# Kernel optimization log

Hardware: AMD Instinct MI355X
Metric: run time of the kernel (lower is better)

The kernel has to match this reference:

```python
import jax, jax.numpy as jnp
import numpy as np

NU, NV, D, H, E = 100000, 50000, 128, 128, 1600000
ALPHA = 0.2  # LeakyReLU slope


def _spmm(rows, cols, vals, x, n_rows):
    # sparse [n_rows, n_cols] @ dense [n_cols, d] via gather + segment_sum
    return jax.ops.segment_sum(vals[:, None] * x[cols], rows, num_segments=n_rows)


def _gcn(x, rows, cols, vals, n_rows, W, b):
    support = x @ W + b  # bias added before spmm is equivalent only if... original adds after spmm
    return None


def _gcn_layer(x, rows, cols, vals, n_rows, W, b):
    support = x @ W
    out = _spmm(rows, cols, vals, support, n_rows) + b
    return jnp.where(out >= 0, out, ALPHA * out)  # LeakyReLU


def _reparam(mean, logstd, noise):
    sigma = jnp.exp(0.1 + 0.9 * jax.nn.softplus(logstd))
    return noise * sigma + mean


def setup_inputs() -> dict:
    key = jax.random.key(0)
    ks = jax.random.split(key, 24)
    stdv = 1.0 / np.sqrt(H)
    u = lambda k, shp, s: jax.random.uniform(k, shp, jnp.float32, -s, s)
    inp = {
        "ufea": jax.random.normal(ks[0], (NU, D), jnp.float32),
        "vfea": jax.random.normal(ks[1], (NV, D), jnp.float32),
        "uv_rows": jax.random.randint(ks[2], (E,), 0, NU, jnp.int32),
        "uv_cols": jax.random.randint(ks[3], (E,), 0, NV, jnp.int32),
        "uv_vals": jax.random.uniform(ks[4], (E,), jnp.float32),
        "vu_rows": jax.random.randint(ks[5], (E,), 0, NV, jnp.int32),
        "vu_cols": jax.random.randint(ks[6], (E,), 0, NU, jnp.int32),
        "vu_vals": jax.random.uniform(ks[7], (E,), jnp.float32),
        "noise_u": jax.random.normal(ks[8], (NU, H), jnp.float32),
        "noise_v": jax.random.normal(ks[9], (NV, H), jnp.float32),
        "gc1_W": u(ks[10], (D, H), stdv), "gc1_b": u(ks[11], (H,), stdv),
        "gc3m_W": u(ks[12], (H, H), stdv), "gc3m_b": u(ks[13], (H,), stdv),
        "gc3s_W": u(ks[14], (H, H), stdv), "gc3s_b": u(ks[15], (H,), stdv),
        "um_W": u(ks[16], (2 * H, H), stdv), "um_b": u(ks[17], (H,), stdv),
        "us_W": u(ks[18], (2 * H, H), stdv), "us_b": u(ks[19], (H,), stdv),
        "im_W": u(ks[20], (2 * H, H), stdv), "im_b": u(ks[21], (H,), stdv),
        "is_W": u(ks[22], (2 * H, H), stdv), "is_b": u(ks[23], (H,), stdv),
    }
    return inp


def reference(ufea, vfea, uv_rows, uv_cols, uv_vals, vu_rows, vu_cols, vu_vals,
              noise_u, noise_v, gc1_W, gc1_b, gc3m_W, gc3m_b, gc3s_W, gc3s_b,
              um_W, um_b, us_W, us_b, im_W, im_b, is_W, is_b):
    nu, nv = ufea.shape[0], vfea.shape[0]
    # user path: VU_adj [nv, nu] then UV_adj [nu, nv]
    user_ho = _gcn_layer(ufea, vu_rows, vu_cols, vu_vals, nv, gc1_W, gc1_b)        # [nv, H]
    user_ho_mean = _gcn_layer(user_ho, uv_rows, uv_cols, uv_vals, nu, gc3m_W, gc3m_b)  # [nu, H]
    user_ho_logstd = _gcn_layer(user_ho, uv_rows, uv_cols, uv_vals, nu, gc3s_W, gc3s_b)
    user_mean = jnp.concatenate((user_ho_mean, ufea), axis=1) @ um_W + um_b
    user_logstd = jnp.concatenate((user_ho_logstd, ufea), axis=1) @ us_W + us_b
    user_z = _reparam(user_mean, user_logstd, noise_u)
    # item path: UV_adj [nu, nv] then VU_adj [nv, nu]
    item_ho = _gcn_layer(vfea, uv_rows, uv_cols, uv_vals, nu, gc1_W, gc1_b)        # [nu, H]
    item_ho_mean = _gcn_layer(item_ho, vu_rows, vu_cols, vu_vals, nv, gc3m_W, gc3m_b)  # [nv, H]
    item_ho_logstd = _gcn_layer(item_ho, vu_rows, vu_cols, vu_vals, nv, gc3s_W, gc3s_b)
    item_mean = jnp.concatenate((item_ho_mean, vfea), axis=1) @ im_W + im_b
    item_logstd = jnp.concatenate((item_ho_logstd, vfea), axis=1) @ is_W + is_b
    item_z = _reparam(item_mean, item_logstd, noise_v)
    return user_z, item_z
```

## Files before the change

kernel.cpp:

```cpp
#include <hip/hip_runtime.h>
#include <math.h>

typedef float f32x4 __attribute__((ext_vector_type(4)));
typedef __bf16 bf16x8 __attribute__((ext_vector_type(8)));
typedef __bf16 bf16x4 __attribute__((ext_vector_type(4)));

#define LRELU_ALPHA 0.2f

__global__ void edge_count(const int* __restrict__ rows, int* __restrict__ cnt, int E) {
    int i = blockIdx.x * 256 + threadIdx.x;
    if (i < E) atomicAdd(&cnt[rows[i]], 1);
}

__global__ __launch_bounds__(512) void scan1(const int* __restrict__ in, int* __restrict__ out,
                                             int* __restrict__ bsum, int ncnt, int nout) {
    __shared__ int s[512];
    int t = threadIdx.x;
    int i = blockIdx.x * 512 + t;
    int v = (i < ncnt) ? in[i] : 0;
    s[t] = v; __syncthreads();
    for (int o = 1; o < 512; o <<= 1) {
        int u = (t >= o) ? s[t - o] : 0;
        __syncthreads();
        s[t] += u;
        __syncthreads();
    }
    if (i < nout) out[i] = s[t] - v;
    if (t == 511) bsum[blockIdx.x] = s[511];
}

__global__ void scan2(int* __restrict__ b, int nb) {
    __shared__ int s[256];
    int t = threadIdx.x;
    int v = (t < nb) ? b[t] : 0;
    s[t] = v; __syncthreads();
    for (int o = 1; o < 256; o <<= 1) {
        int u = (t >= o) ? s[t - o] : 0;
        __syncthreads();
        s[t] += u;
        __syncthreads();
    }
    if (t < nb) b[t] = s[t] - v;
}

__global__ __launch_bounds__(512) void scan3(int* __restrict__ out, const int* __restrict__ bsum, int nout) {
    int i = blockIdx.x * 512 + threadIdx.x;
    if (i < nout) out[i] += bsum[blockIdx.x];
}

__global__ void edge_fill(const int* __restrict__ rows, const int* __restrict__ cols,
                          const float* __restrict__ vals, int* __restrict__ cur,
                          int* __restrict__ ocol, float* __restrict__ oval, int E) {
    int i = blockIdx.x * 256 + threadIdx.x;
    if (i < E) {
        int r = rows[i];
        int p = atomicAdd(&cur[r], 1);
        ocol[p] = cols[i];
        oval[p] = vals[i];
    }
}

__global__ void prep_wt(const float* __restrict__ W, unsigned short* __restrict__ Whi,
                        unsigned short* __restrict__ Wlo, int K) {
    int i = blockIdx.x * 256 + threadIdx.x;
    if (i < K * 128) {
        int k = i >> 7, n = i & 127;
        float f = W[i];
        __bf16 h = (__bf16)f;
        __bf16 l = (__bf16)(f - (float)h);
        Whi[n * K + k] = __builtin_bit_cast(unsigned short, h);
        Wlo[n * K + k] = __builtin_bit_cast(unsigned short, l);
    }
}

__global__ __launch_bounds__(256) void spmm_lrelu(const int* __restrict__ ptr, const int* __restrict__ cols,
                                                  const float* __restrict__ vals, const float* __restrict__ x,
                                                  const float* __restrict__ bias, float* __restrict__ out,
                                                  int nrows) {
    int w = (blockIdx.x << 2) + (threadIdx.x >> 6);
    if (w >= nrows) return;
    int lane = threadIdx.x & 63;
    int s = ptr[w], e = ptr[w + 1];
    const float2* __restrict__ x2 = (const float2*)x;
    float ax = 0.f, ay = 0.f;
    int i = s;
    for (; i + 3 < e; i += 4) {
        int c0 = cols[i], c1 = cols[i + 1], c2 = cols[i + 2], c3 = cols[i + 3];
        float v0 = vals[i], v1 = vals[i + 1], v2 = vals[i + 2], v3 = vals[i + 3];
        float2 g0 = x2[(size_t)c0 * 64 + lane];
        float2 g1 = x2[(size_t)c1 * 64 + lane];
        float2 g2 = x2[(size_t)c2 * 64 + lane];
        float2 g3 = x2[(size_t)c3 * 64 + lane];
        ax += v0 * g0.x + v1 * g1.x + v2 * g2.x + v3 * g3.x;
        ay += v0 * g0.y + v1 * g1.y + v2 * g2.y + v3 * g3.y;
    }
    for (; i < e; i++) {
        int c = cols[i]; float v = vals[i];
        float2 g = x2[(size_t)c * 64 + lane];
        ax += v * g.x; ay += v * g.y;
    }
    float2 b2 = ((const float2*)bias)[lane];
    ax += b2.x; ay += b2.y;
    ax = ax >= 0.f ? ax : LRELU_ALPHA * ax;
    ay = ay >= 0.f ? ay : LRELU_ALPHA * ay;
    float2 o; o.x = ax; o.y = ay;
    ((float2*)out)[(size_t)w * 64 + lane] = o;
}

template <int KT, int EPI>
__global__ __launch_bounds__(256) void gemm128(const float* __restrict__ A1, const float* __restrict__ A2,
                                               const unsigned short* __restrict__ Whi,
                                               const unsigned short* __restrict__ Wlo,
                                               const float* __restrict__ bias,
                                               const float* __restrict__ noise,
                                               float* C, int M) {
    constexpr int K = KT * 64;
    __shared__ __bf16 Ahi[128][72];
    __shared__ __bf16 Alo[128][72];
    __shared__ __bf16 Bhi[128][72];
    __shared__ __bf16 Blo[128][72];
    const int t = threadIdx.x;
    const int lane = t & 63;
    const int w = t >> 6;
    const int wr = w >> 1, wc = w & 1;
    const int l15 = lane & 15, l4 = lane >> 4;
    const int row0 = blockIdx.x * 128;

    f32x4 acc[4][4] = {};

    for (int k0 = 0; k0 < K; k0 += 64) {
        __syncthreads();
        {
            int r = t >> 1, half = t & 1;
            int rg = row0 + r;
            const float* src;
            if constexpr (KT == 2) {
                src = A1 + (size_t)rg * 128 + k0;
            } else {
                src = (k0 < 128) ? (A1 + (size_t)rg * 128 + k0)
                                 : (A2 + (size_t)rg * 128 + (k0 - 128));
            }
#pragma unroll
            for (int q = 0; q < 8; q++) {
                int kk = half * 32 + 4 * q;
                float4 f;
                if (rg < M) f = *(const float4*)(src + kk);
                else        f = make_float4(0.f, 0.f, 0.f, 0.f);
                bf16x4 h, l;
                h[0] = (__bf16)f.x; l[0] = (__bf16)(f.x - (float)h[0]);
                h[1] = (__bf16)f.y; l[1] = (__bf16)(f.y - (float)h[1]);
                h[2] = (__bf16)f.z; l[2] = (__bf16)(f.z - (float)h[2]);
                h[3] = (__bf16)f.w; l[3] = (__bf16)(f.w - (float)h[3]);
                *(bf16x4*)&Ahi[r][kk] = h;
                *(bf16x4*)&Alo[r][kk] = l;
            }
            int n = t >> 1;
            const unsigned short* whsrc = Whi + (size_t)n * K + k0 + half * 32;
            const unsigned short* wlsrc = Wlo + (size_t)n * K + k0 + half * 32;
#pragma unroll
            for (int q = 0; q < 4; q++) {
                uint4 uh = *(const uint4*)(whsrc + 8 * q);
                uint4 ul = *(const uint4*)(wlsrc + 8 * q);
                *(uint4*)&Bhi[n][half * 32 + 8 * q] = uh;
                *(uint4*)&Blo[n][half * 32 + 8 * q] = ul;
            }
        }
        __syncthreads();
#pragma unroll
        for (int kh = 0; kh < 2; kh++) {
            bf16x8 ah[4], al[4], bh[4], bl[4];
#pragma unroll
            for (int mr = 0; mr < 4; mr++) {
                ah[mr] = *(const bf16x8*)&Ahi[wr * 64 + mr * 16 + l15][kh * 32 + l4 * 8];
                al[mr] = *(const bf16x8*)&Alo[wr * 64 + mr * 16 + l15][kh * 32 + l4 * 8];
            }
#pragma unroll
            for (int nc = 0; nc < 4; nc++) {
                bh[nc] = *(const bf16x8*)&Bhi[wc * 64 + nc * 16 + l15][kh * 32 + l4 * 8];
                bl[nc] = *(const bf16x8*)&Blo[wc * 64 + nc * 16 + l15][kh * 32 + l4 * 8];
            }
#pragma unroll
            for (int mr = 0; mr < 4; mr++)
#pragma unroll
                for (int nc = 0; nc < 4; nc++) {
                    acc[mr][nc] = __builtin_amdgcn_mfma_f32_16x16x32_bf16(ah[mr], bh[nc], acc[mr][nc], 0, 0, 0);
                    acc[mr][nc] = __builtin_amdgcn_mfma_f32_16x16x32_bf16(ah[mr], bl[nc], acc[mr][nc], 0, 0, 0);
                    acc[mr][nc] = __builtin_amdgcn_mfma_f32_16x16x32_bf16(al[mr], bh[nc], acc[mr][nc], 0, 0, 0);
                }
        }
    }

#pragma unroll
    for (int mr = 0; mr < 4; mr++) {
        int rowb = row0 + wr * 64 + mr * 16 + l4 * 4;
#pragma unroll
        for (int nc = 0; nc < 4; nc++) {
            int col = wc * 64 + nc * 16 + l15;
#pragma unroll
            for (int j = 0; j < 4; j++) {
                int r = rowb + j;
                if (r < M) {
                    float v = acc[mr][nc][j];
                    if constexpr (EPI == 0) {
                        C[(size_t)r * 128 + col] = v;
                    } else if constexpr (EPI == 1) {
                        C[(size_t)r * 128 + col] = v + bias[col];
                    } else {
                        float mean = v + bias[col];
                        float ls = C[(size_t)r * 128 + col];
                        float sp = ls > 0.f ? ls + log1pf(expf(-ls)) : log1pf(expf(ls));
                        float sg = expf(0.1f + 0.9f * sp);
                        C[(size_t)r * 128 + col] = noise[(size_t)r * 128 + col] * sg + mean;
                    }
                }
            }
        }
    }
}

extern "C" void kernel_launch(void* const* d_in, const int* in_sizes, int n_in,
                              void* d_out, int out_size, void* d_ws, size_t ws_size,
                              hipStream_t stream) {
    const float* ufea    = (const float*)d_in[0];
    const float* vfea    = (const float*)d_in[1];
    const int*   uv_rows = (const int*)d_in[2];
    const int*   uv_cols = (const int*)d_in[3];
    const float* uv_vals = (const float*)d_in[4];
    const int*   vu_rows = (const int*)d_in[5];
    const int*   vu_cols = (const int*)d_in[6];
    const float* vu_vals = (const float*)d_in[7];
    const float* noise_u = (const float*)d_in[8];
    const float* noise_v = (const float*)d_in[9];
    const float* gc1_W  = (const float*)d_in[10];
    const float* gc1_b  = (const float*)d_in[11];
    const float* gc3m_W = (const float*)d_in[12];
    const float* gc3m_b = (const float*)d_in[13];
    const float* gc3s_W = (const float*)d_in[14];
    const float* gc3s_b = (const float*)d_in[15];
    const float* um_W = (const float*)d_in[16];
    const float* um_b = (const float*)d_in[17];
    const float* us_W = (const float*)d_in[18];
    const float* us_b = (const float*)d_in[19];
    const float* im_W = (const float*)d_in[20];
    const float* im_b = (const float*)d_in[21];
    const float* is_W = (const float*)d_in[22];
    const float* is_b = (const float*)d_in[23];

    const int H  = in_sizes[11];
    const int D  = in_sizes[10] / H;
    const int NU = in_sizes[0] / D;
    const int NV = in_sizes[1] / D;
    const int E  = in_sizes[2];

    char* ws = (char*)d_ws;
    size_t off = 0;
    auto alloc = [&](size_t bytes) -> char* {
        char* p = ws + off;
        off = (off + bytes + 255) & ~(size_t)255;
        return p;
    };
    unsigned short* wt_gc1_h  = (unsigned short*)alloc(128 * 128 * 2);
    unsigned short* wt_gc1_l  = (unsigned short*)alloc(128 * 128 * 2);
    unsigned short* wt_gc3m_h = (unsigned short*)alloc(128 * 128 * 2);
    unsigned short* wt_gc3m_l = (unsigned short*)alloc(128 * 128 * 2);
    unsigned short* wt_gc3s_h = (unsigned short*)alloc(128 * 128 * 2);
    unsigned short* wt_gc3s_l = (unsigned short*)alloc(128 * 128 * 2);
    unsigned short* wt_um_h = (unsigned short*)alloc(128 * 256 * 2);
    unsigned short* wt_um_l = (unsigned short*)alloc(128 * 256 * 2);
    unsigned short* wt_us_h = (unsigned short*)alloc(128 * 256 * 2);
    unsigned short* wt_us_l = (unsigned short*)alloc(128 * 256 * 2);
    unsigned short* wt_im_h = (unsigned short*)alloc(128 * 256 * 2);
    unsigned short* wt_im_l = (unsigned short*)alloc(128 * 256 * 2);
    unsigned short* wt_is_h = (unsigned short*)alloc(128 * 256 * 2);
    unsigned short* wt_is_l = (unsigned short*)alloc(128 * 256 * 2);
    int*   ptr_uv = (int*)alloc((size_t)(NU + 1) * 4);
    int*   cur_uv = (int*)alloc((size_t)NU * 4);
    int*   col_uv = (int*)alloc((size_t)E * 4);
    float* val_uv = (float*)alloc((size_t)E * 4);
    int*   ptr_vu = (int*)alloc((size_t)(NV + 1) * 4);
    int*   cur_vu = (int*)alloc((size_t)NV * 4);
    int*   col_vu = (int*)alloc((size_t)E * 4);
    float* val_vu = (float*)alloc((size_t)E * 4);
    int*   bsum   = (int*)alloc(1024 * 4);
    float* bufA = (float*)alloc((size_t)NU * 128 * 4);
    float* bufB = (float*)alloc((size_t)NU * 128 * 4);

    float* outU = (float*)d_out;
    float* outI = outU + (size_t)NU * H;

    const int eb = (E + 255) / 256;
    const int nbU = (NU + 1 + 511) / 512;
    const int nbV = (NV + 1 + 511) / 512;
    const int gU = (NU + 127) / 128, gV = (NV + 127) / 128;
    const int sU = (NU + 3) / 4, sV = (NV + 3) / 4;

    hipMemsetAsync(cur_uv, 0, (size_t)NU * 4, stream);
    hipMemsetAsync(cur_vu, 0, (size_t)NV * 4, stream);
    edge_count<<<eb, 256, 0, stream>>>(uv_rows, cur_uv, E);
    edge_count<<<eb, 256, 0, stream>>>(vu_rows, cur_vu, E);
    scan1<<<nbU, 512, 0, stream>>>(cur_uv, ptr_uv, bsum, NU, NU + 1);
    scan2<<<1, 256, 0, stream>>>(bsum, nbU);
    scan3<<<nbU, 512, 0, stream>>>(ptr_uv, bsum, NU + 1);
    scan1<<<nbV, 512, 0, stream>>>(cur_vu, ptr_vu, bsum, NV, NV + 1);
    scan2<<<1, 256, 0, stream>>>(bsum, nbV);
    scan3<<<nbV, 512, 0, stream>>>(ptr_vu, bsum, NV + 1);
    hipMemcpyAsync(cur_uv, ptr_uv, (size_t)NU * 4, hipMemcpyDeviceToDevice, stream);
    hipMemcpyAsync(cur_vu, ptr_vu, (size_t)NV * 4, hipMemcpyDeviceToDevice, stream);
    edge_fill<<<eb, 256, 0, stream>>>(uv_rows, uv_cols, uv_vals, cur_uv, col_uv, val_uv, E);
    edge_fill<<<eb, 256, 0, stream>>>(vu_rows, vu_cols, vu_vals, cur_vu, col_vu, val_vu, E);

    prep_wt<<<64, 256, 0, stream>>>(gc1_W, wt_gc1_h, wt_gc1_l, 128);
    prep_wt<<<64, 256, 0, stream>>>(gc3m_W, wt_gc3m_h, wt_gc3m_l, 128);
    prep_wt<<<64, 256, 0, stream>>>(gc3s_W, wt_gc3s_h, wt_gc3s_l, 128);
    prep_wt<<<128, 256, 0, stream>>>(um_W, wt_um_h, wt_um_l, 256);
    prep_wt<<<128, 256, 0, stream>>>(us_W, wt_us_h, wt_us_l, 256);
    prep_wt<<<128, 256, 0, stream>>>(im_W, wt_im_h, wt_im_l, 256);
    prep_wt<<<128, 256, 0, stream>>>(is_W, wt_is_h, wt_is_l, 256);

    gemm128<2, 0><<<gU, 256, 0, stream>>>(ufea, nullptr, wt_gc1_h, wt_gc1_l, nullptr, nullptr, bufA, NU);
    spmm_lrelu<<<sV, 256, 0, stream>>>(ptr_vu, col_vu, val_vu, bufA, gc1_b, bufB, NV);
    gemm128<2, 0><<<gV, 256, 0, stream>>>(bufB, nullptr, wt_gc3s_h, wt_gc3s_l, nullptr, nullptr, bufA, NV);
    spmm_lrelu<<<sU, 256, 0, stream>>>(ptr_uv, col_uv, val_uv, bufA, gc3s_b, outU, NU);
    gemm128<4, 1><<<gU, 256, 0, stream>>>(outU, ufea, wt_us_h, wt_us_l, us_b, nullptr, outU, NU);
    gemm128<2, 0><<<gV, 256, 0, stream>>>(bufB, nullptr, wt_gc3m_h, wt_gc3m_l, nullptr, nullptr, bufA, NV);
    spmm_lrelu<<<sU, 256, 0, stream>>>(ptr_uv, col_uv, val_uv, bufA, gc3m_b, bufB, NU);
    gemm128<4, 2><<<gU, 256, 0, stream>>>(bufB, ufea, wt_um_h, wt_um_l, um_b, noise_u, outU, NU);

    gemm128<2, 0><<<gV, 256, 0, stream>>>(vfea, nullptr, wt_gc1_h, wt_gc1_l, nullptr, nullptr, bufA, NV);
    spmm_lrelu<<<sU, 256, 0, stream>>>(ptr_uv, col_uv, val_uv, bufA, gc1_b, bufB, NU);
    gemm128<2, 0><<<gU, 256, 0, stream>>>(bufB, nullptr, wt_gc3s_h, wt_gc3s_l, nullptr, nullptr, bufA, NU);
    spmm_lrelu<<<sV, 256, 0, stream>>>(ptr_vu, col_vu, val_vu, bufA, gc3s_b, outI, NV);
    gemm128<4, 1><<<gV, 256, 0, stream>>>(outI, vfea, wt_is_h, wt_is_l, is_b, nullptr, outI, NV);
    gemm128<2, 0><<<gU, 256, 0, stream>>>(bufB, nullptr, wt_gc3m_h, wt_gc3m_l, nullptr, nullptr, bufA, NU);
    spmm_lrelu<<<sV, 256, 0, stream>>>(ptr_vu, col_vu, val_vu, bufA, gc3m_b, bufB, NV);
    gemm128<4, 2><<<gV, 256, 0, stream>>>(bufB, vfea, wt_im_h, wt_im_l, im_b, noise_v, outI, NV);

    (void)n_in; (void)out_size; (void)ws_size;
}
```

Before: 1.802 ms.

## Replace LDS-tiled GEMM with register-direct MFMA using pre-swizzled weight fragments

Weights are pre-arranged into MFMA fragment order so each lane loads its B operand straight from global memory. The A operand is likewise loaded per lane directly into registers, which removes all shared-memory staging and block barriers. Each wave now computes 32 rows by all 128 columns instead of a 64x64 tile. This drops LDS traffic and syncs, at the cost of redundant weight loads per wave (served from cache) and less coalesced A loads.

```diff
diff --git a/kernel.cpp b/kernel.cpp
--- a/kernel.cpp
+++ b/kernel.cpp
@@ -3,7 +3,6 @@
 
 typedef float f32x4 __attribute__((ext_vector_type(4)));
 typedef __bf16 bf16x8 __attribute__((ext_vector_type(8)));
-typedef __bf16 bf16x4 __attribute__((ext_vector_type(4)));
 
 #define LRELU_ALPHA 0.2f
 
@@ -60,17 +59,21 @@
     }
 }
 
-__global__ void prep_wt(const float* __restrict__ W, unsigned short* __restrict__ Whi,
-                        unsigned short* __restrict__ Wlo, int K) {
-    int i = blockIdx.x * 256 + threadIdx.x;
-    if (i < K * 128) {
-        int k = i >> 7, n = i & 127;
-        float f = W[i];
-        __bf16 h = (__bf16)f;
-        __bf16 l = (__bf16)(f - (float)h);
-        Whi[n * K + k] = __builtin_bit_cast(unsigned short, h);
-        Wlo[n * K + k] = __builtin_bit_cast(unsigned short, l);
-    }
+__global__ void prep_frag(const float* __restrict__ W, unsigned short* __restrict__ Fh,
+                          unsigned short* __restrict__ Fl, int K) {
+    int o = blockIdx.x * 256 + threadIdx.x;
+    if (o >= K * 128) return;
+    int j = o & 7;
+    int lane = (o >> 3) & 63;
+    int blk = o >> 9;
+    int nc = blk & 7, kh = blk >> 3;
+    int col = nc * 16 + (lane & 15);
+    int k = kh * 32 + (lane >> 4) * 8 + j;
+    float f = W[k * 128 + col];
+    __bf16 h = (__bf16)f;
+    __bf16 l = (__bf16)(f - (float)h);
+    Fh[o] = __builtin_bit_cast(unsigned short, h);
+    Fl[o] = __builtin_bit_cast(unsigned short, l);
 }
 
 __global__ __launch_bounds__(256) void spmm_lrelu(const int* __restrict__ ptr, const int* __restrict__ cols,
@@ -107,95 +110,74 @@
     ((float2*)out)[(size_t)w * 64 + lane] = o;
 }
 
-template <int KT, int EPI>
-__global__ __launch_bounds__(256) void gemm128(const float* __restrict__ A1, const float* __restrict__ A2,
-                                               const unsigned short* __restrict__ Whi,
-                                               const unsigned short* __restrict__ Wlo,
-                                               const float* __restrict__ bias,
-                                               const float* __restrict__ noise,
-                                               float* C, int M) {
-    constexpr int K = KT * 64;
-    __shared__ __bf16 Ahi[128][72];
-    __shared__ __bf16 Alo[128][72];
-    __shared__ __bf16 Bhi[128][72];
-    __shared__ __bf16 Blo[128][72];
+template <int KPH, int EPI>
+__global__ __launch_bounds__(256) void gemm_reg(const float* __restrict__ A1, const float* __restrict__ A2,
+                                                const unsigned short* __restrict__ Fh,
+                                                const unsigned short* __restrict__ Fl,
+                                                const float* __restrict__ bias,
+                                                const float* __restrict__ noise,
+                                                float* __restrict__ C, int M) {
     const int t = threadIdx.x;
     const int lane = t & 63;
     const int w = t >> 6;
-    const int wr = w >> 1, wc = w & 1;
     const int l15 = lane & 15, l4 = lane >> 4;
-    const int row0 = blockIdx.x * 128;
-
-    f32x4 acc[4][4] = {};
-
-    for (int k0 = 0; k0 < K; k0 += 64) {
-        __syncthreads();
-        {
-            int r = t >> 1, half = t & 1;
-            int rg = row0 + r;
-            const float* src;
-            if constexpr (KT == 2) {
-                src = A1 + (size_t)rg * 128 + k0;
+    const int row0 = blockIdx.x * 128 + w * 32;
+
+    f32x4 acc[2][8] = {};
+
+#pragma unroll
+    for (int kh = 0; kh < KPH; kh++) {
+        const float* Asrc;
+        int kk;
+        if constexpr (KPH == 8) {
+            Asrc = (kh < 4) ? A1 : A2;
+            kk = (kh & 3) * 32 + l4 * 8;
+        } else {
+            Asrc = A1;
+            kk = kh * 32 + l4 * 8;
+        }
+        bf16x8 ah[2], al[2];
+#pragma unroll
+        for (int mr = 0; mr < 2; mr++) {
+            int r = row0 + mr * 16 + l15;
+            float4 f0, f1;
+            if (r < M) {
+                const float* p = Asrc + (size_t)r * 128 + kk;
+                f0 = *(const float4*)p;
+                f1 = *(const float4*)(p + 4);
             } else {
-                src = (k0 < 128) ? (A1 + (size_t)rg * 128 + k0)
-                                 : (A2 + (size_t)rg * 128 + (k0 - 128));
+                f0 = make_float4(0.f, 0.f, 0.f, 0.f);
+                f1 = f0;
             }
-#pragma unroll
-            for (int q = 0; q < 8; q++) {
-                int kk = half * 32 + 4 * q;
-                float4 f;
-                if (rg < M) f = *(const float4*)(src + kk);
-                else        f = make_float4(0.f, 0.f, 0.f, 0.f);
-                bf16x4 h, l;
-                h[0] = (__bf16)f.x; l[0] = (__bf16)(f.x - (float)h[0]);
-                h[1] = (__bf16)f.y; l[1] = (__bf16)(f.y - (float)h[1]);
-                h[2] = (__bf16)f.z; l[2] = (__bf16)(f.z - (float)h[2]);
-                h[3] = (__bf16)f.w; l[3] = (__bf16)(f.w - (float)h[3]);
-                *(bf16x4*)&Ahi[r][kk] = h;
-                *(bf16x4*)&Alo[r][kk] = l;
-            }
-            int n = t >> 1;
-            const unsigned short* whsrc = Whi + (size_t)n * K + k0 + half * 32;
-            const unsigned short* wlsrc = Wlo + (size_t)n * K + k0 + half * 32;
-#pragma unroll
-            for (int q = 0; q < 4; q++) {
-                uint4 uh = *(const uint4*)(whsrc + 8 * q);
-                uint4 ul = *(const uint4*)(wlsrc + 8 * q);
-                *(uint4*)&Bhi[n][half * 32 + 8 * q] = uh;
-                *(uint4*)&Blo[n][half * 32 + 8 * q] = ul;
+            float fv[8] = {f0.x, f0.y, f0.z, f0.w, f1.x, f1.y, f1.z, f1.w};
+#pragma unroll
+            for (int j = 0; j < 8; j++) {
+                __bf16 h = (__bf16)fv[j];
+                ah[mr][j] = h;
+                al[mr][j] = (__bf16)(fv[j] - (float)h);
             }
         }
-        __syncthreads();
-#pragma unroll
-        for (int kh = 0; kh < 2; kh++) {
-            bf16x8 ah[4], al[4], bh[4], bl[4];
-#pragma unroll
-            for (int mr = 0; mr < 4; mr++) {
-                ah[mr] = *(const bf16x8*)&Ahi[wr * 64 + mr * 16 + l15][kh * 32 + l4 * 8];
-                al[mr] = *(const bf16x8*)&Alo[wr * 64 + mr * 16 + l15][kh * 32 + l4 * 8];
+        const unsigned short* bh_base = Fh + (size_t)kh * 4096;
+        const unsigned short* bl_base = Fl + (size_t)kh * 4096;
+#pragma unroll
+        for (int nc = 0; nc < 8; nc++) {
+            bf16x8 bh = *(const bf16x8*)(bh_base + nc * 512 + lane * 8);
+            bf16x8 bl = *(const bf16x8*)(bl_base + nc * 512 + lane * 8);
+#pragma unroll
+            for (int mr = 0; mr < 2; mr++) {
+                acc[mr][nc] = __builtin_amdgcn_mfma_f32_16x16x32_bf16(ah[mr], bh, acc[mr][nc], 0, 0, 0);
+                acc[mr][nc] = __builtin_amdgcn_mfma_f32_16x16x32_bf16(ah[mr], bl, acc[mr][nc], 0, 0, 0);
+                acc[mr][nc] = __builtin_amdgcn_mfma_f32_16x16x32_bf16(al[mr], bh, acc[mr][nc], 0, 0, 0);
             }
-#pragma unroll
-            for (int nc = 0; nc < 4; nc++) {
-                bh[nc] = *(const bf16x8*)&Bhi[wc * 64 + nc * 16 + l15][kh * 32 + l4 * 8];
-                bl[nc] = *(const bf16x8*)&Blo[wc * 64 + nc * 16 + l15][kh * 32 + l4 * 8];
-            }
-#pragma unroll
-            for (int mr = 0; mr < 4; mr++)
-#pragma unroll
-                for (int nc = 0; nc < 4; nc++) {
-                    acc[mr][nc] = __builtin_amdgcn_mfma_f32_16x16x32_bf16(ah[mr], bh[nc], acc[mr][nc], 0, 0, 0);
-                    acc[mr][nc] = __builtin_amdgcn_mfma_f32_16x16x32_bf16(ah[mr], bl[nc], acc[mr][nc], 0, 0, 0);
-                    acc[mr][nc] = __builtin_amdgcn_mfma_f32_16x16x32_bf16(al[mr], bh[nc], acc[mr][nc], 0, 0, 0);
-                }
         }
     }
 
 #pragma unroll
-    for (int mr = 0; mr < 4; mr++) {
-        int rowb = row0 + wr * 64 + mr * 16 + l4 * 4;
-#pragma unroll
-        for (int nc = 0; nc < 4; nc++) {
-            int col = wc * 64 + nc * 16 + l15;
+    for (int mr = 0; mr < 2; mr++) {
+        int rowb = row0 + mr * 16 + l4 * 4;
+#pragma unroll
+        for (int nc = 0; nc < 8; nc++) {
+            int col = nc * 16 + l15;
 #pragma unroll
             for (int j = 0; j < 4; j++) {
                 int r = rowb + j;
@@ -259,20 +241,20 @@
         off = (off + bytes + 255) & ~(size_t)255;
         return p;
     };
-    unsigned short* wt_gc1_h  = (unsigned short*)alloc(128 * 128 * 2);
-    unsigned short* wt_gc1_l  = (unsigned short*)alloc(128 * 128 * 2);
-    unsigned short* wt_gc3m_h = (unsigned short*)alloc(128 * 128 * 2);
-    unsigned short* wt_gc3m_l = (unsigned short*)alloc(128 * 128 * 2);
-    unsigned short* wt_gc3s_h = (unsigned short*)alloc(128 * 128 * 2);
-    unsigned short* wt_gc3s_l = (unsigned short*)alloc(128 * 128 * 2);
-    unsigned short* wt_um_h = (unsigned short*)alloc(128 * 256 * 2);
-    unsigned short* wt_um_l = (unsigned short*)alloc(128 * 256 * 2);
-    unsigned short* wt_us_h = (unsigned short*)alloc(128 * 256 * 2);
-    unsigned short* wt_us_l = (unsigned short*)alloc(128 * 256 * 2);
-    unsigned short* wt_im_h = (unsigned short*)alloc(128 * 256 * 2);
-    unsigned short* wt_im_l = (unsigned short*)alloc(128 * 256 * 2);
-    unsigned short* wt_is_h = (unsigned short*)alloc(128 * 256 * 2);
-    unsigned short* wt_is_l = (unsigned short*)alloc(128 * 256 * 2);
+    unsigned short* wf_gc1_h  = (unsigned short*)alloc(128 * 128 * 2);
+    unsigned short* wf_gc1_l  = (unsigned short*)alloc(128 * 128 * 2);
+    unsigned short* wf_gc3m_h = (unsigned short*)alloc(128 * 128 * 2);
+    unsigned short* wf_gc3m_l = (unsigned short*)alloc(128 * 128 * 2);
+    unsigned short* wf_gc3s_h = (unsigned short*)alloc(128 * 128 * 2);
+    unsigned short* wf_gc3s_l = (unsigned short*)alloc(128 * 128 * 2);
+    unsigned short* wf_um_h = (unsigned short*)alloc(256 * 128 * 2);
+    unsigned short* wf_um_l = (unsigned short*)alloc(256 * 128 * 2);
+    unsigned short* wf_us_h = (unsigned short*)alloc(256 * 128 * 2);
+    unsigned short* wf_us_l = (unsigned short*)alloc(256 * 128 * 2);
+    unsigned short* wf_im_h = (unsigned short*)alloc(256 * 128 * 2);
+    unsigned short* wf_im_l = (unsigned short*)alloc(256 * 128 * 2);
+    unsigned short* wf_is_h = (unsigned short*)alloc(256 * 128 * 2);
+    unsigned short* wf_is_l = (unsigned short*)alloc(256 * 128 * 2);
     int*   ptr_uv = (int*)alloc((size_t)(NU + 1) * 4);
     int*   cur_uv = (int*)alloc((size_t)NU * 4);
     int*   col_uv = (int*)alloc((size_t)E * 4);
@@ -309,31 +291,31 @@
     edge_fill<<<eb, 256, 0, stream>>>(uv_rows, uv_cols, uv_vals, cur_uv, col_uv, val_uv, E);
     edge_fill<<<eb, 256, 0, stream>>>(vu_rows, vu_cols, vu_vals, cur_vu, col_vu, val_vu, E);
 
-    prep_wt<<<64, 256, 0, stream>>>(gc1_W, wt_gc1_h, wt_gc1_l, 128);
-    prep_wt<<<64, 256, 0, stream>>>(gc3m_W, wt_gc3m_h, wt_gc3m_l, 128);
-    prep_wt<<<64, 256, 0, stream>>>(gc3s_W, wt_gc3s_h, wt_gc3s_l, 128);
-    prep_wt<<<128, 256, 0, stream>>>(um_W, wt_um_h, wt_um_l, 256);
-    prep_wt<<<128, 256, 0, stream>>>(us_W, wt_us_h, wt_us_l, 256);
-    prep_wt<<<128, 256, 0, stream>>>(im_W, wt_im_h, wt_im_l, 256);
-    prep_wt<<<128, 256, 0, stream>>>(is_W, wt_is_h, wt_is_l, 256);
-
-    gemm128<2, 0><<<gU, 256, 0, stream>>>(ufea, nullptr, wt_gc1_h, wt_gc1_l, nullptr, nullptr, bufA, NU);
+    prep_frag<<<64, 256, 0, stream>>>(gc1_W, wf_gc1_h, wf_gc1_l, 128);
+    prep_frag<<<64, 256, 0, stream>>>(gc3m_W, wf_gc3m_h, wf_gc3m_l, 128);
+    prep_frag<<<64, 256, 0, stream>>>(gc3s_W, wf_gc3s_h, wf_gc3s_l, 128);
+    prep_frag<<<128, 256, 0, stream>>>(um_W, wf_um_h, wf_um_l, 256);
+    prep_frag<<<128, 256, 0, stream>>>(us_W, wf_us_h, wf_us_l, 256);
+    prep_frag<<<128, 256, 0, stream>>>(im_W, wf_im_h, wf_im_l, 256);
+    prep_frag<<<128, 256, 0, stream>>>(is_W, wf_is_h, wf_is_l, 256);
+
+    gemm_reg<4, 0><<<gU, 256, 0, stream>>>(ufea, nullptr, wf_gc1_h, wf_gc1_l, nullptr, nullptr, bufA, NU);
     spmm_lrelu<<<sV, 256, 0, stream>>>(ptr_vu, col_vu, val_vu, bufA, gc1_b, bufB, NV);
-    gemm128<2, 0><<<gV, 256, 0, stream>>>(bufB, nullptr, wt_gc3s_h, wt_gc3s_l, nullptr, nullptr, bufA, NV);
+    gemm_reg<4, 0><<<gV, 256, 0, stream>>>(bufB, nullptr, wf_gc3s_h, wf_gc3s_l, nullptr, nullptr, bufA, NV);
     spmm_lrelu<<<sU, 256, 0, stream>>>(ptr_uv, col_uv, val_uv, bufA, gc3s_b, outU, NU);
-    gemm128<4, 1><<<gU, 256, 0, stream>>>(outU, ufea, wt_us_h, wt_us_l, us_b, nullptr, outU, NU);
-    gemm128<2, 0><<<gV, 256, 0, stream>>>(bufB, nullptr, wt_gc3m_h, wt_gc3m_l, nullptr, nullptr, bufA, NV);
+    gemm_reg<8, 1><<<gU, 256, 0, stream>>>(outU, ufea, wf_us_h, wf_us_l, us_b, nullptr, outU, NU);
+    gemm_reg<4, 0><<<gV, 256, 0, stream>>>(bufB, nullptr, wf_gc3m_h, wf_gc3m_l, nullptr, nullptr, bufA, NV);
     spmm_lrelu<<<sU, 256, 0, stream>>>(ptr_uv, col_uv, val_uv, bufA, gc3m_b, bufB, NU);
-    gemm128<4, 2><<<gU, 256, 0, stream>>>(bufB, ufea, wt_um_h, wt_um_l, um_b, noise_u, outU, NU);
-
-    gemm128<2, 0><<<gV, 256, 0, stream>>>(vfea, nullptr, wt_gc1_h, wt_gc1_l, nullptr, nullptr, bufA, NV);
+    gemm_reg<8, 2><<<gU, 256, 0, stream>>>(bufB, ufea, wf_um_h, wf_um_l, um_b, noise_u, outU, NU);
+
+    gemm_reg<4, 0><<<gV, 256, 0, stream>>>(vfea, nullptr, wf_gc1_h, wf_gc1_l, nullptr, nullptr, bufA, NV);
     spmm_lrelu<<<sU, 256, 0, stream>>>(ptr_uv, col_uv, val_uv, bufA, gc1_b, bufB, NU);
-    gemm128<2, 0><<<gU, 256, 0, stream>>>(bufB, nullptr, wt_gc3s_h, wt_gc3s_l, nullptr, nullptr, bufA, NU);
+    gemm_reg<4, 0><<<gU, 256, 0, stream>>>(bufB, nullptr, wf_gc3s_h, wf_gc3s_l, nullptr, nullptr, bufA, NU);
     spmm_lrelu<<<sV, 256, 0, stream>>>(ptr_vu, col_vu, val_vu, bufA, gc3s_b, outI, NV);
-    gemm128<4, 1><<<gV, 256, 0, stream>>>(outI, vfea, wt_is_h, wt_is_l, is_b, nullptr, outI, NV);
-    gemm128<2, 0><<<gU, 256, 0, stream>>>(bufB, nullptr, wt_gc3m_h, wt_gc3m_l, nullptr, nullptr, bufA, NU);
+    gemm_reg<8, 1><<<gV, 256, 0, stream>>>(outI, vfea, wf_is_h, wf_is_l, is_b, nullptr, outI, NV);
+    gemm_reg<4, 0><<<gU, 256, 0, stream>>>(bufB, nullptr, wf_gc3m_h, wf_gc3m_l, nullptr, nullptr, bufA, NU);
     spmm_lrelu<<<sV, 256, 0, stream>>>(ptr_vu, col_vu, val_vu, bufA, gc3m_b, bufB, NV);
-    gemm128<4, 2><<<gV, 256, 0, stream>>>(bufB, vfea, wt_im_h, wt_im_l, im_b, noise_v, outI, NV);
+    gemm_reg<8, 2><<<gV, 256, 0, stream>>>(bufB, vfea, wf_im_h, wf_im_l, im_b, noise_v, outI, NV);
 
     (void)n_in; (void)out_size; (void)ws_size;
 }
```

After: 1.832 ms. Within noise of the previous version (+1.7%).
